# Optimization experiments

Hardware: AMD Instinct MI355X
Metric: run time of the kernel (lower is better)

The kernel has to match this reference:

```python
import jax, jax.numpy as jnp
import numpy as np

R = 3          # bilateral radius -> 7x7 window (kernel_size=7, dilation=1)
NIC = 12       # num_input_channels per frame
NHS = 1        # num_hidden_states
DN = ('NCHW', 'OIHW', 'NCHW')


def _conv(x, w, b, groups=1):
    y = jax.lax.conv_general_dilated(x, w, (1, 1), 'SAME',
                                     dimension_numbers=DN,
                                     feature_group_count=groups)
    return y + b[None, :, None, None]


def _lcn(x, k=3):
    # run_lcn(color, 3): local contrast normalization with k x k box window, per channel
    C = x.shape[1]
    box = jnp.ones((C, 1, k, k), x.dtype) / (k * k)
    zb = jnp.zeros((C,), x.dtype)
    mean = _conv(x, box, zb, groups=C)
    mean2 = _conv(x * x, box, zb, groups=C)
    var = jnp.maximum(mean2 - mean * mean, 0.0)
    return (x - mean) * jax.lax.rsqrt(var + 1e-5)


def _bilateral(dyn, feat, scale):
    # cross-bilateral: weights from guide features, applied to dynamic channels
    B, _, H, W = dyn.shape
    pad = ((0, 0), (0, 0), (R, R), (R, R))
    fp = jnp.pad(feat, pad, mode='edge')
    dp = jnp.pad(dyn, pad, mode='edge')
    s = scale[None, :, None, None]            # [1,8,1,1] per-feature inverse sigma^2
    acc = jnp.zeros_like(dyn)
    wsum = jnp.zeros((B, 1, H, W), dyn.dtype)
    for dy in range(2 * R + 1):
        for dx in range(2 * R + 1):
            fq = fp[:, :, dy:dy + H, dx:dx + W]
            w = jnp.exp(-jnp.sum(s * (feat - fq) ** 2, axis=1, keepdims=True))
            acc = acc + w * dp[:, :, dy:dy + H, dx:dx + W]
            wsum = wsum + w
    return acc / (wsum + 1e-8)


def _forward(x, alpha, cr_w0, cr_b0, cr_w1, cr_b1, cr_w2, cr_b2,
             hs_w0, hs_b0, hs_w1, hs_b1, hs_w2, hs_b2,
             filt_w, filt_b, filt_scale):
    B, CT, H, W = x.shape
    num_frames = CT // NIC
    a = alpha[0]
    temporal = jnp.zeros((B, 3 + NHS, H, W), x.dtype)
    outs = []
    for i in range(num_frames):
        frame = x[:, i * NIC:(i + 1) * NIC]
        color, albedo, fixed = frame[:, :3], frame[:, 3:6], frame[:, 3:]
        rec_in = jnp.concatenate([_lcn(color), color], axis=1)           # 6ch
        h = jax.nn.relu(_conv(rec_in, cr_w0, cr_b0))
        h = jax.nn.relu(_conv(h, cr_w1, cr_b1))
        recombined = _conv(h, cr_w2, cr_b2)                              # 3ch
        hs_in = jnp.concatenate([recombined, fixed], axis=1)             # 12ch
        h = jax.nn.relu(_conv(hs_in, hs_w0, hs_b0))
        h = jax.nn.relu(_conv(h, hs_w1, hs_b1))
        hidden = _conv(h, hs_w2, hs_b2)                                  # 1ch
        dynamic = jnp.concatenate([color, hidden], axis=1)               # 4ch
        if i != 0:
            dynamic = a * dynamic + (1.0 - a) * temporal
        filtered = jnp.concatenate([dynamic, fixed], axis=1)             # 13ch
        for k in range(5):
            feat = _conv(filtered, filt_w[k], filt_b[k])                 # 8 guide features
            fdyn = _bilateral(filtered[:, :3 + NHS], feat, filt_scale[k])
            filtered = jnp.concatenate([fdyn, fixed], axis=1)
        outs.append(albedo * filtered[:, :3])
        temporal = filtered[:, :3 + NHS]
    return jnp.concatenate(outs, axis=1)   # [B, 3*num_frames, H, W]


def setup_inputs():
    key = jax.random.key(0)
    ks = jax.random.split(key, 12)
    w = lambda k, s: (0.1 * jax.random.normal(k, s)).astype(jnp.float32)
    z = lambda s: jnp.zeros(s, jnp.float32)
    return {
        'x': jax.random.normal(ks[0], (1, 48, 720, 1280), dtype=jnp.float32),
        'alpha': jnp.full((1,), 0.5, jnp.float32),
        'cr_w0': w(ks[1], (6, 6, 3, 3)),   'cr_b0': z((6,)),
        'cr_w1': w(ks[2], (12, 6, 3, 3)),  'cr_b1': z((12,)),
        'cr_w2': w(ks[3], (3, 12, 3, 3)),  'cr_b2': z((3,)),
        'hs_w0': w(ks[4], (12, 12, 3, 3)), 'hs_b0': z((12,)),
        'hs_w1': w(ks[5], (12, 12, 3, 3)), 'hs_b1': z((12,)),
        'hs_w2': w(ks[6], (1, 12, 3, 3)),  'hs_b2': z((1,)),
        'filt_w': w(ks[7], (5, 8, 13, 3, 3)), 'filt_b': z((5, 8)),
        'filt_scale': 0.5 * jax.random.uniform(ks[8], (5, 8), dtype=jnp.float32),
    }


def reference(x, alpha, cr_w0, cr_b0, cr_w1, cr_b1, cr_w2, cr_b2,
              hs_w0, hs_b0, hs_w1, hs_b1, hs_w2, hs_b2,
              filt_w, filt_b, filt_scale):
    return _forward(x, alpha, cr_w0, cr_b0, cr_w1, cr_b1, cr_w2, cr_b2,
                    hs_w0, hs_b0, hs_w1, hs_b1, hs_w2, hs_b2,
                    filt_w, filt_b, filt_scale)
```

## Files before the change

kernel.cpp:

```cpp
#include <hip/hip_runtime.h>

#define HH 720
#define WW 1280
#define HWP (HH*WW)

static constexpr int NFRM = 4;
typedef _Float16 h2 __attribute__((ext_vector_type(2)));

__device__ __forceinline__ unsigned pkh(float a, float b) {
  return __builtin_bit_cast(unsigned, __builtin_amdgcn_cvt_pkrtz(a, b));
}
__device__ __forceinline__ int bswz(int lin) { return lin ^ ((lin >> 3) & 7); }

template <int C0, int C1, int COUT, bool RELU>
__global__ __launch_bounds__(256) void conv3x3_v4(const float* __restrict__ in0, long i0fs,
                                                  const float* __restrict__ in1, long i1fs,
                                                  const float* __restrict__ w,
                                                  const float* __restrict__ b,
                                                  float* __restrict__ out, long ofs) {
  constexpr int PX = 4;
  constexpr int CIN = C0 + C1;
  constexpr int NBX = WW / 64;
  int fi = blockIdx.y;
  in0 += (size_t)fi * i0fs;
  out += (size_t)fi * ofs;
  const float* in1f = nullptr;
  if constexpr (C1 > 0) in1f = in1 + (size_t)fi * i1fs;

  int bx = blockIdx.x % NBX;
  int by = blockIdx.x / NBX;
  int tx = threadIdx.x & 15;
  int ty = threadIdx.x >> 4;
  int gx0 = bx * 64 + tx * PX;
  int gy  = by * 16 + ty;

  float acc[COUT][PX];
  #pragma unroll
  for (int co = 0; co < COUT; ++co) {
    float bv = b[co];
    #pragma unroll
    for (int px = 0; px < PX; ++px) acc[co][px] = bv;
  }

  const bool lok = (gx0 > 0);
  const bool rok = (gx0 + PX < WW);

  for (int c = 0; c < CIN; ++c) {
    const float* ch;
    if constexpr (C1 > 0)
      ch = (c < C0) ? (in0 + (size_t)c * HWP) : (in1f + (size_t)(c - C0) * HWP);
    else
      ch = in0 + (size_t)c * HWP;
    float r[3][PX + 2];
    #pragma unroll
    for (int ky = 0; ky < 3; ++ky) {
      int iy = gy + ky - 1;
      bool yok = (iy >= 0) && (iy < HH);
      const float* row = ch + (ptrdiff_t)iy * WW;
      float4 a = yok ? *reinterpret_cast<const float4*>(row + gx0)
                     : make_float4(0.f, 0.f, 0.f, 0.f);
      r[ky][1] = a.x; r[ky][2] = a.y; r[ky][3] = a.z; r[ky][4] = a.w;
      r[ky][0]      = (yok && lok) ? row[gx0 - 1]  : 0.f;
      r[ky][PX + 1] = (yok && rok) ? row[gx0 + PX] : 0.f;
    }
    #pragma unroll
    for (int co = 0; co < COUT; ++co) {
      #pragma unroll
      for (int ky = 0; ky < 3; ++ky) {
        #pragma unroll
        for (int kx = 0; kx < 3; ++kx) {
          float wv = w[((co * CIN + c) * 3 + ky) * 3 + kx];
          #pragma unroll
          for (int px = 0; px < PX; ++px)
            acc[co][px] = fmaf(wv, r[ky][px + kx], acc[co][px]);
        }
      }
    }
  }

  size_t p = (size_t)gy * WW + gx0;
  #pragma unroll
  for (int co = 0; co < COUT; ++co) {
    float4 o;
    o.x = RELU ? fmaxf(acc[co][0], 0.f) : acc[co][0];
    o.y = RELU ? fmaxf(acc[co][1], 0.f) : acc[co][1];
    o.z = RELU ? fmaxf(acc[co][2], 0.f) : acc[co][2];
    o.w = RELU ? fmaxf(acc[co][3], 0.f) : acc[co][3];
    *reinterpret_cast<float4*>(out + (size_t)co * HWP + p) = o;
  }
}

__global__ __launch_bounds__(128) void lcn_v3(const float* __restrict__ x, long ifs,
                                              float* __restrict__ out, long ofs) {
  constexpr int NBX = WW / 128;
  int fi = blockIdx.y;
  const float* color = x + (size_t)fi * ifs;
  out += (size_t)fi * ofs;
  int bx = blockIdx.x % NBX;
  int by = blockIdx.x / NBX;
  int tx = threadIdx.x & 15;
  int ty = threadIdx.x >> 4;
  int gx0 = bx * 128 + tx * 8;
  int gy  = by * 8 + ty;
  const bool lok = (gx0 > 0);
  const bool rok = (gx0 + 8 < WW);
  size_t p = (size_t)gy * WW + gx0;

  #pragma unroll
  for (int c = 0; c < 3; ++c) {
    const float* ch = color + (size_t)c * HWP;
    float r[3][10];
    #pragma unroll
    for (int ky = 0; ky < 3; ++ky) {
      int iy = gy + ky - 1;
      bool yok = (iy >= 0) && (iy < HH);
      const float* row = ch + (ptrdiff_t)iy * WW;
      float4 a = yok ? *reinterpret_cast<const float4*>(row + gx0)
                     : make_float4(0.f, 0.f, 0.f, 0.f);
      float4 q = yok ? *reinterpret_cast<const float4*>(row + gx0 + 4)
                     : make_float4(0.f, 0.f, 0.f, 0.f);
      r[ky][0] = (yok && lok) ? row[gx0 - 1] : 0.f;
      r[ky][1] = a.x; r[ky][2] = a.y; r[ky][3] = a.z; r[ky][4] = a.w;
      r[ky][5] = q.x; r[ky][6] = q.y; r[ky][7] = q.z; r[ky][8] = q.w;
      r[ky][9] = (yok && rok) ? row[gx0 + 8] : 0.f;
    }
    float lcnv[8], cv[8];
    #pragma unroll
    for (int px = 0; px < 8; ++px) {
      float s = 0.f, s2 = 0.f;
      #pragma unroll
      for (int ky = 0; ky < 3; ++ky)
        #pragma unroll
        for (int kx = 0; kx < 3; ++kx) {
          float v = r[ky][px + kx];
          s += v; s2 = fmaf(v, v, s2);
        }
      float mean = s * (1.f / 9.f);
      float mean2 = s2 * (1.f / 9.f);
      float var = fmaxf(mean2 - mean * mean, 0.f);
      cv[px] = r[1][px + 1];
      lcnv[px] = (cv[px] - mean) * rsqrtf(var + 1e-5f);
    }
    #pragma unroll
    for (int h = 0; h < 2; ++h) {
      float4 o0 = make_float4(lcnv[4*h+0], lcnv[4*h+1], lcnv[4*h+2], lcnv[4*h+3]);
      float4 o1 = make_float4(cv[4*h+0], cv[4*h+1], cv[4*h+2], cv[4*h+3]);
      *reinterpret_cast<float4*>(out + (size_t)c * HWP + p + 4*h) = o0;
      *reinterpret_cast<float4*>(out + (size_t)(3 + c) * HWP + p + 4*h) = o1;
    }
  }
}

__global__ __launch_bounds__(256) void blend_v3(const float* __restrict__ color,
                                                const float* __restrict__ hid,
                                                const float* __restrict__ temporal,
                                                const float* __restrict__ alpha,
                                                float* __restrict__ dyn, int first) {
  int i = (blockIdx.x * 256 + threadIdx.x) * 4;
  if (i >= HWP) return;
  if (first) {
    #pragma unroll
    for (int c = 0; c < 3; ++c)
      *reinterpret_cast<float4*>(dyn + (size_t)c * HWP + i) =
          *reinterpret_cast<const float4*>(color + (size_t)c * HWP + i);
    *reinterpret_cast<float4*>(dyn + 3 * (size_t)HWP + i) =
        *reinterpret_cast<const float4*>(hid + i);
  } else {
    float a = alpha[0];
    float om = 1.f - a;
    #pragma unroll
    for (int c = 0; c < 4; ++c) {
      const float* src = (c < 3) ? (color + (size_t)c * HWP) : hid;
      float4 cv = *reinterpret_cast<const float4*>(src + i);
      float4 tv = *reinterpret_cast<const float4*>(temporal + (size_t)c * HWP + i);
      float4 o;
      o.x = a * cv.x + om * tv.x;
      o.y = a * cv.y + om * tv.y;
      o.z = a * cv.z + om * tv.z;
      o.w = a * cv.w + om * tv.w;
      *reinterpret_cast<float4*>(dyn + (size_t)c * HWP + i) = o;
    }
  }
}

#define BC 38
#define BR 22
#define BNPX (BC*BR)
#define BPAD 840

template <bool OUT>
__global__ __launch_bounds__(256, 4) void bilateral_v5(const float* __restrict__ dyn,
                                                       const float* __restrict__ feat,
                                                       const float* __restrict__ scale,
                                                       float* __restrict__ outdyn,
                                                       const float* __restrict__ albedo,
                                                       float* __restrict__ outp) {
  __shared__ uint4  ft[BPAD];
  __shared__ float4 dt[BPAD];
  int bx = blockIdx.x % 40;
  int by = blockIdx.x / 40;
  int tid = threadIdx.x;

  for (int i = tid; i < BNPX; i += 256) {
    int py = i / BC;
    int px = i - py * BC;
    int gy = min(max(by * 16 + py - 3, 0), HH - 1);
    int gx = min(max(bx * 32 + px - 3, 0), WW - 1);
    size_t g = (size_t)gy * WW + gx;
    int w = bswz(i);
    dt[w] = make_float4(dyn[g], dyn[HWP + g], dyn[2*(size_t)HWP + g], dyn[3*(size_t)HWP + g]);
    uint4 u;
    u.x = pkh(feat[g],                 feat[HWP + g]);
    u.y = pkh(feat[2*(size_t)HWP + g], feat[3*(size_t)HWP + g]);
    u.z = pkh(feat[4*(size_t)HWP + g], feat[5*(size_t)HWP + g]);
    u.w = pkh(feat[6*(size_t)HWP + g], feat[7*(size_t)HWP + g]);
    ft[w] = u;
  }
  __syncthreads();

  int txg = tid & 15;
  int ty  = tid >> 4;

  float sv[8];
  #pragma unroll
  for (int c = 0; c < 8; ++c) sv[c] = scale[c];

  float sfc[2][8], A[2];
  #pragma unroll
  for (int p = 0; p < 2; ++p) {
    int lin = (ty + 3) * BC + txg * 2 + 3 + p;
    uint4 u = ft[bswz(lin)];
    h2 a0 = __builtin_bit_cast(h2, u.x), a1 = __builtin_bit_cast(h2, u.y);
    h2 a2 = __builtin_bit_cast(h2, u.z), a3 = __builtin_bit_cast(h2, u.w);
    float fc[8] = {(float)a0[0], (float)a0[1], (float)a1[0], (float)a1[1],
                   (float)a2[0], (float)a2[1], (float)a3[0], (float)a3[1]};
    float aa = 0.f;
    #pragma unroll
    for (int c = 0; c < 8; ++c) {
      sfc[p][c] = sv[c] * fc[c];
      aa = fmaf(sfc[p][c], fc[c], aa);
    }
    A[p] = aa;
  }

  float acc[2][4], ws2[2];
  #pragma unroll
  for (int p = 0; p < 2; ++p) {
    ws2[p] = 0.f;
    acc[p][0] = acc[p][1] = acc[p][2] = acc[p][3] = 0.f;
  }

  for (int dy = 0; dy < 7; ++dy) {
    int rowb = (ty + dy) * BC + txg * 2;
    #pragma unroll
    for (int dx = 0; dx < 8; ++dx) {
      int w = bswz(rowb + dx);
      float4 dv = dt[w];
      uint4 u = ft[w];
      h2 a0 = __builtin_bit_cast(h2, u.x), a1 = __builtin_bit_cast(h2, u.y);
      h2 a2 = __builtin_bit_cast(h2, u.z), a3 = __builtin_bit_cast(h2, u.w);
      float f[8] = {(float)a0[0], (float)a0[1], (float)a1[0], (float)a1[1],
                    (float)a2[0], (float)a2[1], (float)a3[0], (float)a3[1]};
      float B = 0.f;
      #pragma unroll
      for (int c = 0; c < 8; ++c) B = fmaf(sv[c] * f[c], f[c], B);
      #pragma unroll
      for (int p = 0; p < 2; ++p) {
        if (dx - p >= 0 && dx - p <= 6) {
          float C = 0.f;
          #pragma unroll
          for (int c = 0; c < 8; ++c) C = fmaf(sfc[p][c], f[c], C);
          float e = fmaf(-2.f, C, A[p] + B);
          float wgt = __expf(-e);
          acc[p][0] = fmaf(wgt, dv.x, acc[p][0]);
          acc[p][1] = fmaf(wgt, dv.y, acc[p][1]);
          acc[p][2] = fmaf(wgt, dv.z, acc[p][2]);
          acc[p][3] = fmaf(wgt, dv.w, acc[p][3]);
          ws2[p] += wgt;
        }
      }
    }
  }

  int gy = by * 16 + ty;
  int gx0 = bx * 32 + txg * 2;
  size_t p0 = (size_t)gy * WW + gx0;
  float inv0 = 1.f / (ws2[0] + 1e-8f);
  float inv1 = 1.f / (ws2[1] + 1e-8f);
  #pragma unroll
  for (int c = 0; c < 4; ++c) {
    float2 o = make_float2(acc[0][c] * inv0, acc[1][c] * inv1);
    *reinterpret_cast<float2*>(outdyn + (size_t)c * HWP + p0) = o;
    if (OUT && c < 3) {
      float2 al = *reinterpret_cast<const float2*>(albedo + (size_t)c * HWP + p0);
      float2 oo = make_float2(o.x * al.x, o.y * al.y);
      *reinterpret_cast<float2*>(outp + (size_t)c * HWP + p0) = oo;
    }
  }
}

extern "C" void kernel_launch(void* const* d_in, const int* in_sizes, int n_in,
                              void* d_out, int out_size, void* d_ws, size_t ws_size,
                              hipStream_t stream) {
  const float* x          = (const float*)d_in[0];
  const float* alpha      = (const float*)d_in[1];
  const float* cr_w0      = (const float*)d_in[2];
  const float* cr_b0      = (const float*)d_in[3];
  const float* cr_w1      = (const float*)d_in[4];
  const float* cr_b1      = (const float*)d_in[5];
  const float* cr_w2      = (const float*)d_in[6];
  const float* cr_b2      = (const float*)d_in[7];
  const float* hs_w0      = (const float*)d_in[8];
  const float* hs_b0      = (const float*)d_in[9];
  const float* hs_w1      = (const float*)d_in[10];
  const float* hs_b1      = (const float*)d_in[11];
  const float* hs_w2      = (const float*)d_in[12];
  const float* hs_b2      = (const float*)d_in[13];
  const float* filt_w     = (const float*)d_in[14];
  const float* filt_b     = (const float*)d_in[15];
  const float* filt_scale = (const float*)d_in[16];

  float* out = (float*)d_out;
  float* ws  = (float*)d_ws;
  const size_t P = (size_t)HWP;

  bool batched = ws_size >= (size_t)108 * P * sizeof(float);
  float *bufA, *bufB, *dynT, *dynA, *dynB, *hid, *feat;
  if (batched) {
    bufA = ws;            bufB = ws + 48 * P;
    dynT = ws + 96 * P;   dynA = ws + 100 * P;  dynB = ws + 104 * P;
  } else {
    bufA = ws;            bufB = ws + 12 * P;
    dynT = ws + 24 * P;   dynA = ws + 28 * P;   dynB = ws + 32 * P;
  }
  hid  = bufA;
  feat = bufB;

  const int NB8 = (WW / 128) * (HH / 8);
  const int NBC = (WW / 64)  * (HH / 16);
  const int NBE = HWP / (256 * 4);
  const int NBB = (WW / 32)  * (HH / 16);

  if (batched) {
    dim3 g8(NB8, NFRM), gc(NBC, NFRM);
    lcn_v3<<<g8, 128, 0, stream>>>(x, 12 * P, bufA, 6 * P);
    conv3x3_v4<6, 0, 6,  true ><<<gc, 256, 0, stream>>>(bufA, 6 * P,  nullptr, 0, cr_w0, cr_b0, bufB, 6 * P);
    conv3x3_v4<6, 0, 12, true ><<<gc, 256, 0, stream>>>(bufB, 6 * P,  nullptr, 0, cr_w1, cr_b1, bufA, 12 * P);
    conv3x3_v4<12, 0, 3, false><<<gc, 256, 0, stream>>>(bufA, 12 * P, nullptr, 0, cr_w2, cr_b2, bufB, 3 * P);
    conv3x3_v4<3, 9, 12, true ><<<gc, 256, 0, stream>>>(bufB, 3 * P,  x + 3 * P, 12 * P, hs_w0, hs_b0, bufA, 12 * P);
    conv3x3_v4<12, 0, 12, true><<<gc, 256, 0, stream>>>(bufA, 12 * P, nullptr, 0, hs_w1, hs_b1, bufB, 12 * P);
    conv3x3_v4<12, 0, 1, false><<<gc, 256, 0, stream>>>(bufB, 12 * P, nullptr, 0, hs_w2, hs_b2, hid, P);
  }

  for (int f = 0; f < NFRM; ++f) {
    const float* frame  = x + (size_t)f * 12 * P;
    const float* fixedp = frame + 3 * P;

    if (!batched) {
      dim3 g8(NB8, 1), gc(NBC, 1);
      lcn_v3<<<g8, 128, 0, stream>>>(frame, 0, bufA, 0);
      conv3x3_v4<6, 0, 6,  true ><<<gc, 256, 0, stream>>>(bufA, 0, nullptr, 0, cr_w0, cr_b0, bufB, 0);
      conv3x3_v4<6, 0, 12, true ><<<gc, 256, 0, stream>>>(bufB, 0, nullptr, 0, cr_w1, cr_b1, bufA, 0);
      conv3x3_v4<12, 0, 3, false><<<gc, 256, 0, stream>>>(bufA, 0, nullptr, 0, cr_w2, cr_b2, bufB, 0);
      conv3x3_v4<3, 9, 12, true ><<<gc, 256, 0, stream>>>(bufB, 0, fixedp, 0, hs_w0, hs_b0, bufA, 0);
      conv3x3_v4<12, 0, 12, true><<<gc, 256, 0, stream>>>(bufA, 0, nullptr, 0, hs_w1, hs_b1, bufB, 0);
      conv3x3_v4<12, 0, 1, false><<<gc, 256, 0, stream>>>(bufB, 0, nullptr, 0, hs_w2, hs_b2, hid, 0);
    }

    const float* hidf = batched ? (hid + (size_t)f * P) : hid;
    blend_v3<<<NBE, 256, 0, stream>>>(frame, hidf, dynT, alpha, dynA, f == 0 ? 1 : 0);

    float* cur = dynA;
    float* nxt = dynB;
    for (int k = 0; k < 5; ++k) {
      conv3x3_v4<4, 9, 8, false><<<dim3(NBC, 1), 256, 0, stream>>>(
          cur, 0, fixedp, 0, filt_w + (size_t)k * 8 * 13 * 9, filt_b + k * 8, feat, 0);
      const float* sk = filt_scale + k * 8;
      if (k < 4) {
        bilateral_v5<false><<<NBB, 256, 0, stream>>>(cur, feat, sk, nxt, nullptr, nullptr);
        float* t = cur; cur = nxt; nxt = t;
      } else {
        bilateral_v5<true><<<NBB, 256, 0, stream>>>(cur, feat, sk, dynT,
                                                    fixedp, out + (size_t)f * 3 * P);
      }
    }
  }
}
```

Baseline: 2.547 ms.

## Store CNN intermediate activations as packed fp16 to cut memory traffic

The LCN output and all recurrent/hidden-state CNN intermediates are now stored as packed half-precision pairs instead of fp32. A new conv kernel reads fp16 inputs and writes fp16 outputs, and the blend kernel decodes the fp16 hidden state. This halves the bandwidth and workspace for those stages at the cost of fp16 rounding in intermediates. The bilateral kernel's occupancy hint also rises from 4 to 6 blocks, which could force register spills.

```diff
diff --git a/kernel.cpp b/kernel.cpp
--- a/kernel.cpp
+++ b/kernel.cpp
@@ -3,6 +3,8 @@
 #define HH 720
 #define WW 1280
 #define HWP (HH*WW)
+#define HPW (WW/2)
+#define HP  (HWP/2)
 
 static constexpr int NFRM = 4;
 typedef _Float16 h2 __attribute__((ext_vector_type(2)));
@@ -11,14 +13,15 @@
   return __builtin_bit_cast(unsigned, __builtin_amdgcn_cvt_pkrtz(a, b));
 }
 __device__ __forceinline__ int bswz(int lin) { return lin ^ ((lin >> 3) & 7); }
+__device__ __forceinline__ float lo16(unsigned u) { h2 v = __builtin_bit_cast(h2, u); return (float)v[0]; }
+__device__ __forceinline__ float hi16(unsigned u) { h2 v = __builtin_bit_cast(h2, u); return (float)v[1]; }
 
 template <int C0, int C1, int COUT, bool RELU>
-__global__ __launch_bounds__(256) void conv3x3_v4(const float* __restrict__ in0, long i0fs,
-                                                  const float* __restrict__ in1, long i1fs,
-                                                  const float* __restrict__ w,
-                                                  const float* __restrict__ b,
-                                                  float* __restrict__ out, long ofs) {
-  constexpr int PX = 4;
+__global__ __launch_bounds__(256) void conv_pp(const unsigned* __restrict__ in0, long i0fs,
+                                               const float* __restrict__ in1, long i1fs,
+                                               const float* __restrict__ w,
+                                               const float* __restrict__ b,
+                                               unsigned* __restrict__ out, long ofs) {
   constexpr int CIN = C0 + C1;
   constexpr int NBX = WW / 64;
   int fi = blockIdx.y;
@@ -31,6 +34,107 @@
   int by = blockIdx.x / NBX;
   int tx = threadIdx.x & 15;
   int ty = threadIdx.x >> 4;
+  int gx0 = bx * 64 + tx * 4;
+  int gy  = by * 16 + ty;
+  int D   = gx0 >> 1;
+
+  float acc[COUT][4];
+  #pragma unroll
+  for (int co = 0; co < COUT; ++co) {
+    float bv = b[co];
+    #pragma unroll
+    for (int px = 0; px < 4; ++px) acc[co][px] = bv;
+  }
+
+  const bool lok = (gx0 > 0);
+  const bool rok = (gx0 + 4 < WW);
+
+  float r[3][6];
+  for (int c = 0; c < C0; ++c) {
+    const unsigned* ch = in0 + (size_t)c * HP;
+    #pragma unroll
+    for (int ky = 0; ky < 3; ++ky) {
+      int iy = gy + ky - 1;
+      bool yok = (iy >= 0) && (iy < HH);
+      const unsigned* row = ch + (ptrdiff_t)iy * HPW;
+      unsigned um = (yok && lok) ? row[D - 1] : 0u;
+      uint2 uc = yok ? *reinterpret_cast<const uint2*>(row + D) : make_uint2(0u, 0u);
+      unsigned up = (yok && rok) ? row[D + 2] : 0u;
+      r[ky][0] = hi16(um);
+      r[ky][1] = lo16(uc.x); r[ky][2] = hi16(uc.x);
+      r[ky][3] = lo16(uc.y); r[ky][4] = hi16(uc.y);
+      r[ky][5] = lo16(up);
+    }
+    #pragma unroll
+    for (int co = 0; co < COUT; ++co) {
+      #pragma unroll
+      for (int ky = 0; ky < 3; ++ky) {
+        #pragma unroll
+        for (int kx = 0; kx < 3; ++kx) {
+          float wv = w[((co * CIN + c) * 3 + ky) * 3 + kx];
+          #pragma unroll
+          for (int px = 0; px < 4; ++px)
+            acc[co][px] = fmaf(wv, r[ky][px + kx], acc[co][px]);
+        }
+      }
+    }
+  }
+  if constexpr (C1 > 0) {
+    for (int c = 0; c < C1; ++c) {
+      const float* ch = in1f + (size_t)c * HWP;
+      #pragma unroll
+      for (int ky = 0; ky < 3; ++ky) {
+        int iy = gy + ky - 1;
+        bool yok = (iy >= 0) && (iy < HH);
+        const float* row = ch + (ptrdiff_t)iy * WW;
+        float4 a = yok ? *reinterpret_cast<const float4*>(row + gx0)
+                       : make_float4(0.f, 0.f, 0.f, 0.f);
+        r[ky][1] = a.x; r[ky][2] = a.y; r[ky][3] = a.z; r[ky][4] = a.w;
+        r[ky][0] = (yok && lok) ? row[gx0 - 1] : 0.f;
+        r[ky][5] = (yok && rok) ? row[gx0 + 4] : 0.f;
+      }
+      int cw = C0 + c;
+      #pragma unroll
+      for (int co = 0; co < COUT; ++co) {
+        #pragma unroll
+        for (int ky = 0; ky < 3; ++ky) {
+          #pragma unroll
+          for (int kx = 0; kx < 3; ++kx) {
+            float wv = w[((co * CIN + cw) * 3 + ky) * 3 + kx];
+            #pragma unroll
+            for (int px = 0; px < 4; ++px)
+              acc[co][px] = fmaf(wv, r[ky][px + kx], acc[co][px]);
+          }
+        }
+      }
+    }
+  }
+
+  size_t pD = (size_t)gy * HPW + D;
+  #pragma unroll
+  for (int co = 0; co < COUT; ++co) {
+    float o0 = RELU ? fmaxf(acc[co][0], 0.f) : acc[co][0];
+    float o1 = RELU ? fmaxf(acc[co][1], 0.f) : acc[co][1];
+    float o2 = RELU ? fmaxf(acc[co][2], 0.f) : acc[co][2];
+    float o3 = RELU ? fmaxf(acc[co][3], 0.f) : acc[co][3];
+    uint2 o; o.x = pkh(o0, o1); o.y = pkh(o2, o3);
+    *reinterpret_cast<uint2*>(out + (size_t)co * HP + pD) = o;
+  }
+}
+
+template <int C0, int C1, int COUT, bool RELU>
+__global__ __launch_bounds__(256) void conv3x3_v4(const float* __restrict__ in0,
+                                                  const float* __restrict__ in1,
+                                                  const float* __restrict__ w,
+                                                  const float* __restrict__ b,
+                                                  float* __restrict__ out) {
+  constexpr int PX = 4;
+  constexpr int CIN = C0 + C1;
+  constexpr int NBX = WW / 64;
+  int bx = blockIdx.x % NBX;
+  int by = blockIdx.x / NBX;
+  int tx = threadIdx.x & 15;
+  int ty = threadIdx.x >> 4;
   int gx0 = bx * 64 + tx * PX;
   int gy  = by * 16 + ty;
 
@@ -46,11 +150,7 @@
   const bool rok = (gx0 + PX < WW);
 
   for (int c = 0; c < CIN; ++c) {
-    const float* ch;
-    if constexpr (C1 > 0)
-      ch = (c < C0) ? (in0 + (size_t)c * HWP) : (in1f + (size_t)(c - C0) * HWP);
-    else
-      ch = in0 + (size_t)c * HWP;
+    const float* ch = (c < C0) ? (in0 + (size_t)c * HWP) : (in1 + (size_t)(c - C0) * HWP);
     float r[3][PX + 2];
     #pragma unroll
     for (int ky = 0; ky < 3; ++ky) {
@@ -90,8 +190,8 @@
   }
 }
 
-__global__ __launch_bounds__(128) void lcn_v3(const float* __restrict__ x, long ifs,
-                                              float* __restrict__ out, long ofs) {
+__global__ __launch_bounds__(128) void lcn_p(const float* __restrict__ x, long ifs,
+                                             unsigned* __restrict__ out, long ofs) {
   constexpr int NBX = WW / 128;
   int fi = blockIdx.y;
   const float* color = x + (size_t)fi * ifs;
@@ -104,7 +204,7 @@
   int gy  = by * 8 + ty;
   const bool lok = (gx0 > 0);
   const bool rok = (gx0 + 8 < WW);
-  size_t p = (size_t)gy * WW + gx0;
+  size_t pD = (size_t)gy * HPW + (gx0 >> 1);
 
   #pragma unroll
   for (int c = 0; c < 3; ++c) {
@@ -141,37 +241,37 @@
       cv[px] = r[1][px + 1];
       lcnv[px] = (cv[px] - mean) * rsqrtf(var + 1e-5f);
     }
-    #pragma unroll
-    for (int h = 0; h < 2; ++h) {
-      float4 o0 = make_float4(lcnv[4*h+0], lcnv[4*h+1], lcnv[4*h+2], lcnv[4*h+3]);
-      float4 o1 = make_float4(cv[4*h+0], cv[4*h+1], cv[4*h+2], cv[4*h+3]);
-      *reinterpret_cast<float4*>(out + (size_t)c * HWP + p + 4*h) = o0;
-      *reinterpret_cast<float4*>(out + (size_t)(3 + c) * HWP + p + 4*h) = o1;
-    }
-  }
-}
-
-__global__ __launch_bounds__(256) void blend_v3(const float* __restrict__ color,
-                                                const float* __restrict__ hid,
+    uint4 u0, u1;
+    u0.x = pkh(lcnv[0], lcnv[1]); u0.y = pkh(lcnv[2], lcnv[3]);
+    u0.z = pkh(lcnv[4], lcnv[5]); u0.w = pkh(lcnv[6], lcnv[7]);
+    u1.x = pkh(cv[0], cv[1]);     u1.y = pkh(cv[2], cv[3]);
+    u1.z = pkh(cv[4], cv[5]);     u1.w = pkh(cv[6], cv[7]);
+    *reinterpret_cast<uint4*>(out + (size_t)c * HP + pD) = u0;
+    *reinterpret_cast<uint4*>(out + (size_t)(3 + c) * HP + pD) = u1;
+  }
+}
+
+__global__ __launch_bounds__(256) void blend_v5(const float* __restrict__ color,
+                                                const unsigned* __restrict__ hid,
                                                 const float* __restrict__ temporal,
                                                 const float* __restrict__ alpha,
                                                 float* __restrict__ dyn, int first) {
   int i = (blockIdx.x * 256 + threadIdx.x) * 4;
   if (i >= HWP) return;
+  uint2 hu = *reinterpret_cast<const uint2*>(hid + (i >> 1));
+  float4 hv = make_float4(lo16(hu.x), hi16(hu.x), lo16(hu.y), hi16(hu.y));
   if (first) {
     #pragma unroll
     for (int c = 0; c < 3; ++c)
       *reinterpret_cast<float4*>(dyn + (size_t)c * HWP + i) =
           *reinterpret_cast<const float4*>(color + (size_t)c * HWP + i);
-    *reinterpret_cast<float4*>(dyn + 3 * (size_t)HWP + i) =
-        *reinterpret_cast<const float4*>(hid + i);
+    *reinterpret_cast<float4*>(dyn + 3 * (size_t)HWP + i) = hv;
   } else {
     float a = alpha[0];
     float om = 1.f - a;
     #pragma unroll
     for (int c = 0; c < 4; ++c) {
-      const float* src = (c < 3) ? (color + (size_t)c * HWP) : hid;
-      float4 cv = *reinterpret_cast<const float4*>(src + i);
+      float4 cv = (c < 3) ? *reinterpret_cast<const float4*>(color + (size_t)c * HWP + i) : hv;
       float4 tv = *reinterpret_cast<const float4*>(temporal + (size_t)c * HWP + i);
       float4 o;
       o.x = a * cv.x + om * tv.x;
@@ -189,7 +289,7 @@
 #define BPAD 840
 
 template <bool OUT>
-__global__ __launch_bounds__(256, 4) void bilateral_v5(const float* __restrict__ dyn,
+__global__ __launch_bounds__(256, 6) void bilateral_v5(const float* __restrict__ dyn,
                                                        const float* __restrict__ feat,
                                                        const float* __restrict__ scale,
                                                        float* __restrict__ outdyn,
@@ -230,10 +330,8 @@
   for (int p = 0; p < 2; ++p) {
     int lin = (ty + 3) * BC + txg * 2 + 3 + p;
     uint4 u = ft[bswz(lin)];
-    h2 a0 = __builtin_bit_cast(h2, u.x), a1 = __builtin_bit_cast(h2, u.y);
-    h2 a2 = __builtin_bit_cast(h2, u.z), a3 = __builtin_bit_cast(h2, u.w);
-    float fc[8] = {(float)a0[0], (float)a0[1], (float)a1[0], (float)a1[1],
-                   (float)a2[0], (float)a2[1], (float)a3[0], (float)a3[1]};
+    float fc[8] = {lo16(u.x), hi16(u.x), lo16(u.y), hi16(u.y),
+                   lo16(u.z), hi16(u.z), lo16(u.w), hi16(u.w)};
     float aa = 0.f;
     #pragma unroll
     for (int c = 0; c < 8; ++c) {
@@ -257,10 +355,8 @@
       int w = bswz(rowb + dx);
       float4 dv = dt[w];
       uint4 u = ft[w];
-      h2 a0 = __builtin_bit_cast(h2, u.x), a1 = __builtin_bit_cast(h2, u.y);
-      h2 a2 = __builtin_bit_cast(h2, u.z), a3 = __builtin_bit_cast(h2, u.w);
-      float f[8] = {(float)a0[0], (float)a0[1], (float)a1[0], (float)a1[1],
-                    (float)a2[0], (float)a2[1], (float)a3[0], (float)a3[1]};
+      float f[8] = {lo16(u.x), hi16(u.x), lo16(u.y), hi16(u.y),
+                    lo16(u.z), hi16(u.z), lo16(u.w), hi16(u.w)};
       float B = 0.f;
       #pragma unroll
       for (int c = 0; c < 8; ++c) B = fmaf(sv[c] * f[c], f[c], B);
@@ -324,57 +420,61 @@
   float* ws  = (float*)d_ws;
   const size_t P = (size_t)HWP;
 
-  bool batched = ws_size >= (size_t)108 * P * sizeof(float);
-  float *bufA, *bufB, *dynT, *dynA, *dynB, *hid, *feat;
+  bool batched = ws_size >= (size_t)68 * P * sizeof(float);
+  unsigned *pA, *pB;
+  float *dynT, *dynA, *dynB, *feat;
   if (batched) {
-    bufA = ws;            bufB = ws + 48 * P;
-    dynT = ws + 96 * P;   dynA = ws + 100 * P;  dynB = ws + 104 * P;
+    pA = (unsigned*)ws;
+    pB = (unsigned*)(ws + 24 * P);
+    dynT = ws + 48 * P;  dynA = ws + 52 * P;  dynB = ws + 56 * P;
+    feat = ws + 60 * P;
   } else {
-    bufA = ws;            bufB = ws + 12 * P;
-    dynT = ws + 24 * P;   dynA = ws + 28 * P;   dynB = ws + 32 * P;
-  }
-  hid  = bufA;
-  feat = bufB;
+    pA = (unsigned*)ws;
+    pB = (unsigned*)(ws + 6 * P);
+    dynT = ws + 12 * P;  dynA = ws + 16 * P;  dynB = ws + 20 * P;
+    feat = ws + 24 * P;
+  }
+  unsigned* hid = pA;
 
   const int NB8 = (WW / 128) * (HH / 8);
   const int NBC = (WW / 64)  * (HH / 16);
   const int NBE = HWP / (256 * 4);
   const int NBB = (WW / 32)  * (HH / 16);
 
-  if (batched) {
-    dim3 g8(NB8, NFRM), gc(NBC, NFRM);
-    lcn_v3<<<g8, 128, 0, stream>>>(x, 12 * P, bufA, 6 * P);
-    conv3x3_v4<6, 0, 6,  true ><<<gc, 256, 0, stream>>>(bufA, 6 * P,  nullptr, 0, cr_w0, cr_b0, bufB, 6 * P);
-    conv3x3_v4<6, 0, 12, true ><<<gc, 256, 0, stream>>>(bufB, 6 * P,  nullptr, 0, cr_w1, cr_b1, bufA, 12 * P);
-    conv3x3_v4<12, 0, 3, false><<<gc, 256, 0, stream>>>(bufA, 12 * P, nullptr, 0, cr_w2, cr_b2, bufB, 3 * P);
-    conv3x3_v4<3, 9, 12, true ><<<gc, 256, 0, stream>>>(bufB, 3 * P,  x + 3 * P, 12 * P, hs_w0, hs_b0, bufA, 12 * P);
-    conv3x3_v4<12, 0, 12, true><<<gc, 256, 0, stream>>>(bufA, 12 * P, nullptr, 0, hs_w1, hs_b1, bufB, 12 * P);
-    conv3x3_v4<12, 0, 1, false><<<gc, 256, 0, stream>>>(bufB, 12 * P, nullptr, 0, hs_w2, hs_b2, hid, P);
-  }
+  const int NF = batched ? NFRM : 1;
+  dim3 g8(NB8, NF), gc(NBC, NF);
+  long xs   = batched ? 12 * (long)P : 0;
+  long s6   = batched ? 6  * (long)HP : 0;
+  long s12  = batched ? 12 * (long)HP : 0;
+  long s3   = batched ? 3  * (long)HP : 0;
+  long s1   = batched ? (long)HP : 0;
+
+  auto run_cnn = [&](const float* xin) {
+    lcn_p<<<g8, 128, 0, stream>>>(xin, xs, pA, s6);
+    conv_pp<6, 0, 6,  true ><<<gc, 256, 0, stream>>>(pA, s6,  nullptr, 0, cr_w0, cr_b0, pB, s6);
+    conv_pp<6, 0, 12, true ><<<gc, 256, 0, stream>>>(pB, s6,  nullptr, 0, cr_w1, cr_b1, pA, s12);
+    conv_pp<12, 0, 3, false><<<gc, 256, 0, stream>>>(pA, s12, nullptr, 0, cr_w2, cr_b2, pB, s3);
+    conv_pp<3, 9, 12, true ><<<gc, 256, 0, stream>>>(pB, s3,  xin + 3 * P, xs, hs_w0, hs_b0, pA, s12);
+    conv_pp<12, 0, 12, true><<<gc, 256, 0, stream>>>(pA, s12, nullptr, 0, hs_w1, hs_b1, pB, s12);
+    conv_pp<12, 0, 1, false><<<gc, 256, 0, stream>>>(pB, s12, nullptr, 0, hs_w2, hs_b2, pA, s1);
+  };
+
+  if (batched) run_cnn(x);
 
   for (int f = 0; f < NFRM; ++f) {
     const float* frame  = x + (size_t)f * 12 * P;
     const float* fixedp = frame + 3 * P;
 
-    if (!batched) {
-      dim3 g8(NB8, 1), gc(NBC, 1);
-      lcn_v3<<<g8, 128, 0, stream>>>(frame, 0, bufA, 0);
-      conv3x3_v4<6, 0, 6,  true ><<<gc, 256, 0, stream>>>(bufA, 0, nullptr, 0, cr_w0, cr_b0, bufB, 0);
-      conv3x3_v4<6, 0, 12, true ><<<gc, 256, 0, stream>>>(bufB, 0, nullptr, 0, cr_w1, cr_b1, bufA, 0);
-      conv3x3_v4<12, 0, 3, false><<<gc, 256, 0, stream>>>(bufA, 0, nullptr, 0, cr_w2, cr_b2, bufB, 0);
-      conv3x3_v4<3, 9, 12, true ><<<gc, 256, 0, stream>>>(bufB, 0, fixedp, 0, hs_w0, hs_b0, bufA, 0);
-      conv3x3_v4<12, 0, 12, true><<<gc, 256, 0, stream>>>(bufA, 0, nullptr, 0, hs_w1, hs_b1, bufB, 0);
-      conv3x3_v4<12, 0, 1, false><<<gc, 256, 0, stream>>>(bufB, 0, nullptr, 0, hs_w2, hs_b2, hid, 0);
-    }
-
-    const float* hidf = batched ? (hid + (size_t)f * P) : hid;
-    blend_v3<<<NBE, 256, 0, stream>>>(frame, hidf, dynT, alpha, dynA, f == 0 ? 1 : 0);
+    if (!batched) run_cnn(frame);
+
+    const unsigned* hidf = batched ? (hid + (size_t)f * HP) : hid;
+    blend_v5<<<NBE, 256, 0, stream>>>(frame, hidf, dynT, alpha, dynA, f == 0 ? 1 : 0);
 
     float* cur = dynA;
     float* nxt = dynB;
     for (int k = 0; k < 5; ++k) {
       conv3x3_v4<4, 9, 8, false><<<dim3(NBC, 1), 256, 0, stream>>>(
-          cur, 0, fixedp, 0, filt_w + (size_t)k * 8 * 13 * 9, filt_b + k * 8, feat, 0);
+          cur, fixedp, filt_w + (size_t)k * 8 * 13 * 9, filt_b + k * 8, feat);
       const float* sk = filt_scale + k * 8;
       if (k < 4) {
         bilateral_v5<false><<<NBB, 256, 0, stream>>>(cur, feat, sk, nxt, nullptr, nullptr);
```

Result: slower. 2.683 ms (+5.3%).
